# Performance work log

Measured on AMD Instinct MI355X. Metric: run time of the kernel, lower is better.

The kernel has to match this reference:

```python
import jax, jax.numpy as jnp
import numpy as np

D = 1024   # embedding_dim
H = 16     # head_num
DH = D // H
STD = 0.02


def setup_inputs() -> dict:
    key = jax.random.key(0)
    ks = jax.random.split(key, 8)
    B, S = 16, 2048
    inp = {
        "hidden_states": jax.random.normal(ks[0], (B, S, D), dtype=jnp.float32),
        "attention_mask": jnp.zeros((B, 1, S), dtype=jnp.float32),
        # nn.Linear params, stored as [in, out] for direct matmul
        "Wq": jax.random.normal(ks[1], (D, D), dtype=jnp.float32) * STD,
        "bq": jnp.zeros((D,), dtype=jnp.float32),
        "Wqa": jax.random.normal(ks[2], (D, H), dtype=jnp.float32) * STD,
        "bqa": jnp.zeros((H,), dtype=jnp.float32),
        "Wk": jax.random.normal(ks[3], (D, D), dtype=jnp.float32) * STD,
        "bk": jnp.zeros((D,), dtype=jnp.float32),
        "Wka": jax.random.normal(ks[4], (D, H), dtype=jnp.float32) * STD,
        "bka": jnp.zeros((H,), dtype=jnp.float32),
        "Wt": jax.random.normal(ks[5], (D, D), dtype=jnp.float32) * STD,
        "bt": jnp.zeros((D,), dtype=jnp.float32),
    }
    return inp


def reference(hidden_states, attention_mask, Wq, bq, Wqa, bqa, Wk, bk, Wka, bka, Wt, bt):
    B, S, _ = hidden_states.shape
    scale = 1.0 / np.sqrt(DH).astype(np.float32)

    mixed_q = hidden_states @ Wq + bq          # [B,S,D]
    mixed_k = hidden_states @ Wk + bk          # [B,S,D]

    # per-head query pooling scores: [B,S,H] -> [B,H,S]
    q_score = jnp.transpose(mixed_q @ Wqa + bqa, (0, 2, 1)) * scale + attention_mask
    q_weight = jax.nn.softmax(q_score, axis=-1)                 # [B,H,S]

    q_layer = mixed_q.reshape(B, S, H, DH).transpose(0, 2, 1, 3)  # [B,H,S,dh]
    pooled_q = jnp.einsum('bhs,bhsd->bhd', q_weight, q_layer)     # [B,H,dh]
    pooled_q_flat = pooled_q.reshape(B, 1, D)                     # [B,1,D] (head-major)

    # elementwise modulate keys with pooled query (broadcast, no repeat)
    mixed_qk = mixed_k * pooled_q_flat                            # [B,S,D]

    qk_score = jnp.transpose(mixed_qk @ Wka + bka, (0, 2, 1)) * scale + attention_mask
    qk_weight = jax.nn.softmax(qk_score, axis=-1)                 # [B,H,S]

    k_layer = mixed_qk.reshape(B, S, H, DH).transpose(0, 2, 1, 3)  # [B,H,S,dh]
    pooled_k = jnp.einsum('bhs,bhsd->bhd', qk_weight, k_layer)     # [B,H,dh]

    weighted = pooled_k[:, :, None, :] * q_layer                   # [B,H,S,dh]
    weighted = weighted.transpose(0, 2, 1, 3).reshape(B, S, D)     # [B,S,D]

    return weighted @ Wt + bt + mixed_q
```

## Files before the change

### kernel.cpp

```cpp
#include <hip/hip_runtime.h>
#include <hip/hip_bf16.h>
#include <stdint.h>

#define D_ 1024
#define H_ 16
#define DH_ 64
#define S_ 2048
#define B_ 16
static constexpr float SCALE = 0.125f;

typedef __bf16 bf16_t;
typedef __bf16 bf16x8 __attribute__((ext_vector_type(8)));
typedef __bf16 bf16x4 __attribute__((ext_vector_type(4)));
typedef float  f32x4  __attribute__((ext_vector_type(4)));

__device__ __forceinline__ void llds16(const void* g, void* l) {
  __builtin_amdgcn_global_load_lds(
      (const __attribute__((address_space(1))) void*)g,
      (__attribute__((address_space(3))) void*)l, 16, 0, 0);
}

__global__ __launch_bounds__(256)
void f32_to_bf16(const float* __restrict__ src, bf16_t* __restrict__ dst) {
  size_t base = ((size_t)blockIdx.x * 256 + threadIdx.x) * 8;
  f32x4 a = *(const f32x4*)&src[base];
  f32x4 b = *(const f32x4*)&src[base + 4];
  bf16x8 o;
#pragma unroll
  for (int i = 0; i < 4; ++i) { o[i] = (bf16_t)a[i]; o[4 + i] = (bf16_t)b[i]; }
  *(bf16x8*)&dst[base] = o;
}

__global__ __launch_bounds__(256)
void transpose1024_all(const float* __restrict__ s0, const float* __restrict__ s1,
                       const float* __restrict__ s2, bf16_t* __restrict__ d0,
                       bf16_t* __restrict__ d1, bf16_t* __restrict__ d2) {
  __shared__ bf16_t t[64][65];
  const float* src = (blockIdx.z == 0) ? s0 : (blockIdx.z == 1) ? s1 : s2;
  bf16_t* dst      = (blockIdx.z == 0) ? d0 : (blockIdx.z == 1) ? d1 : d2;
  const int n0 = blockIdx.x * 64, k0 = blockIdx.y * 64;
  const int r = threadIdx.x >> 4, c4 = (threadIdx.x & 15) * 4;
#pragma unroll
  for (int p = 0; p < 4; ++p) {
    int row = p * 16 + r;
    f32x4 f = *(const f32x4*)&src[(size_t)(k0 + row) * 1024 + n0 + c4];
#pragma unroll
    for (int i = 0; i < 4; ++i) t[row][c4 + i] = (bf16_t)f[i];
  }
  __syncthreads();
#pragma unroll
  for (int p = 0; p < 4; ++p) {
    int row = p * 16 + r;
    bf16x4 v;
#pragma unroll
    for (int i = 0; i < 4; ++i) v[i] = t[c4 + i][row];
    *(bf16x4*)&dst[(size_t)(n0 + row) * 1024 + k0 + c4] = v;
  }
}

__global__ __launch_bounds__(256)
void transpose_small_all(const float* __restrict__ sa, const float* __restrict__ sb,
                         bf16_t* __restrict__ da, bf16_t* __restrict__ db) {
  int g = blockIdx.x * 256 + threadIdx.x;
  const float* src = (g < 1024) ? sa : sb;
  bf16_t* dst      = (g < 1024) ? da : db;
  int k = g & 1023;
#pragma unroll
  for (int h = 0; h < H_; ++h) dst[h * 1024 + k] = (bf16_t)src[k * H_ + h];
}

__global__ __launch_bounds__(256, 2)
void gemm_qk(const bf16_t* __restrict__ A, const bf16_t* __restrict__ WqT,
             const bf16_t* __restrict__ WkT, const float* __restrict__ bq,
             const float* __restrict__ bk, bf16_t* __restrict__ mq,
             bf16_t* __restrict__ mk) {
  constexpr int K = 1024, N = 1024;
  __shared__ __align__(16) bf16_t lA[128 * 32];
  __shared__ __align__(16) bf16_t lB[128 * 32];
  __shared__ __align__(16) float est[4][16 * 68];
  const int tid = threadIdx.x;
  const int lane = tid & 63, wid = tid >> 6;
  const int wr = wid >> 1, wc = wid & 1;

  const int wgid = (blockIdx.x & 7) * 512 + (blockIdx.x >> 3);
  const int m0 = (wgid >> 4) * 128;
  const int nsel = wgid & 15;
  const int n0 = (nsel & 7) * 128;
  const bf16_t* BT = (nsel < 8) ? WqT : WkT;
  const float* bias = (nsel < 8) ? bq : bk;
  bf16_t* Cout = (nsel < 8) ? mq : mk;

  const int ar = lane & 15;
  const int kq = lane >> 4;

  int rowc[2], colc[2], dstoff[2];
#pragma unroll
  for (int j = 0; j < 2; ++j) {
    int c = j * 256 + tid;
    int row = c >> 2, s = c & 3;
    rowc[j] = row;
    colc[j] = (((s - (row >> 1)) & 3) << 3);
    dstoff[j] = c * 8;
  }

  f32x4 acc[4][4] = {};

  for (int k0 = 0; k0 < K; k0 += 32) {
#pragma unroll
    for (int j = 0; j < 2; ++j) {
      llds16(BT + (size_t)(n0 + rowc[j]) * K + k0 + colc[j], lB + dstoff[j]);
      llds16(A + (size_t)(m0 + rowc[j]) * K + k0 + colc[j], lA + dstoff[j]);
    }
    __syncthreads();
    bf16x8 af[4], bg[4];
#pragma unroll
    for (int m = 0; m < 4; ++m) {
      int r = wr * 64 + m * 16 + ar;
      af[m] = *(const bf16x8*)&lA[r * 32 + (((kq + (r >> 1)) & 3) << 3)];
    }
#pragma unroll
    for (int n = 0; n < 4; ++n) {
      int r = wc * 64 + n * 16 + ar;
      bg[n] = *(const bf16x8*)&lB[r * 32 + (((kq + (r >> 1)) & 3) << 3)];
    }
#pragma unroll
    for (int m = 0; m < 4; ++m)
#pragma unroll
      for (int n = 0; n < 4; ++n)
        acc[m][n] = __builtin_amdgcn_mfma_f32_16x16x32_bf16(af[m], bg[n], acc[m][n], 0, 0, 0);
    __syncthreads();
  }

  float* st = est[wid];
  const int erow = lane >> 2;
  const int ecol = (lane & 3) * 16;
  const int gcb = n0 + wc * 64;
  const int qrow = (lane >> 4) * 4;
  const int qcol = lane & 15;
  f32x4 bb[4];
#pragma unroll
  for (int q = 0; q < 4; ++q) bb[q] = *(const f32x4*)&bias[gcb + ecol + q * 4];
#pragma unroll
  for (int m = 0; m < 4; ++m) {
#pragma unroll
    for (int n = 0; n < 4; ++n)
#pragma unroll
      for (int j = 0; j < 4; ++j)
        st[(qrow + j) * 68 + n * 16 + qcol] = acc[m][n][j];
    asm volatile("s_waitcnt lgkmcnt(0)" ::: "memory");
    __builtin_amdgcn_sched_barrier(0);
    const int grow = m0 + wr * 64 + m * 16 + erow;
    f32x4 v[4];
#pragma unroll
    for (int q = 0; q < 4; ++q) v[q] = *(f32x4*)&st[erow * 68 + ecol + q * 4];
#pragma unroll
    for (int q = 0; q < 4; ++q)
#pragma unroll
      for (int i = 0; i < 4; ++i) v[q][i] += bb[q][i];
    bf16x8 o0, o1;
#pragma unroll
    for (int i = 0; i < 4; ++i) { o0[i] = (bf16_t)v[0][i]; o0[4 + i] = (bf16_t)v[1][i]; }
#pragma unroll
    for (int i = 0; i < 4; ++i) { o1[i] = (bf16_t)v[2][i]; o1[4 + i] = (bf16_t)v[3][i]; }
    bf16_t* op = Cout + (size_t)grow * N + gcb + ecol;
    *(bf16x8*)&op[0] = o0;
    *(bf16x8*)&op[8] = o1;
  }
}

__global__ __launch_bounds__(256, 2)
void gemm_out(const bf16_t* __restrict__ A, const bf16_t* __restrict__ BT,
              const float* __restrict__ bias, float* __restrict__ Cout,
              const bf16_t* __restrict__ resid, const float* __restrict__ pkA) {
  constexpr int K = 1024, N = 1024;
  __shared__ __align__(16) bf16_t lA[128 * 32];
  __shared__ __align__(16) bf16_t lB[128 * 32];
  __shared__ __align__(16) float est[4][16 * 68];
  const int tid = threadIdx.x;
  const int lane = tid & 63, wid = tid >> 6;
  const int wr = wid >> 1, wc = wid & 1;

  const int wgid = (blockIdx.x & 7) * 256 + (blockIdx.x >> 3);
  const int m0 = (wgid >> 3) * 128;
  const int n0 = (wgid & 7) * 128;
  const int b = m0 / S_;

  const int ar = lane & 15;
  const int kq = lane >> 4;

  int rowc[2], colc[2], dstoff[2];
#pragma unroll
  for (int j = 0; j < 2; ++j) {
    int c = j * 256 + tid;
    int row = c >> 2, s = c & 3;
    rowc[j] = row;
    colc[j] = (((s - (row >> 1)) & 3) << 3);
    dstoff[j] = c * 8;
  }

  f32x4 acc[4][4] = {};

  for (int k0 = 0; k0 < K; k0 += 32) {
#pragma unroll
    for (int j = 0; j < 2; ++j) {
      llds16(BT + (size_t)(n0 + rowc[j]) * K + k0 + colc[j], lB + dstoff[j]);
      bf16x8 v = *(const bf16x8*)(A + (size_t)(m0 + rowc[j]) * K + k0 + colc[j]);
      const float* pkp = pkA + b * D_ + k0 + colc[j];
      f32x4 p0 = *(const f32x4*)pkp;
      f32x4 p1 = *(const f32x4*)(pkp + 4);
      bf16x8 o;
#pragma unroll
      for (int i = 0; i < 4; ++i) {
        o[i]     = (bf16_t)((float)v[i] * p0[i]);
        o[4 + i] = (bf16_t)((float)v[4 + i] * p1[i]);
      }
      *(bf16x8*)&lA[dstoff[j]] = o;
    }
    __syncthreads();
    bf16x8 af[4], bg[4];
#pragma unroll
    for (int m = 0; m < 4; ++m) {
      int r = wr * 64 + m * 16 + ar;
      af[m] = *(const bf16x8*)&lA[r * 32 + (((kq + (r >> 1)) & 3) << 3)];
    }
#pragma unroll
    for (int n = 0; n < 4; ++n) {
      int r = wc * 64 + n * 16 + ar;
      bg[n] = *(const bf16x8*)&lB[r * 32 + (((kq + (r >> 1)) & 3) << 3)];
    }
#pragma unroll
    for (int m = 0; m < 4; ++m)
#pragma unroll
      for (int n = 0; n < 4; ++n)
        acc[m][n] = __builtin_amdgcn_mfma_f32_16x16x32_bf16(af[m], bg[n], acc[m][n], 0, 0, 0);
    __syncthreads();
  }

  float* st = est[wid];
  const int erow = lane >> 2;
  const int ecol = (lane & 3) * 16;
  const int gcb = n0 + wc * 64;
  const int qrow = (lane >> 4) * 4;
  const int qcol = lane & 15;
  f32x4 bb[4];
#pragma unroll
  for (int q = 0; q < 4; ++q) bb[q] = *(const f32x4*)&bias[gcb + ecol + q * 4];
#pragma unroll
  for (int m = 0; m < 4; ++m) {
#pragma unroll
    for (int n = 0; n < 4; ++n)
#pragma unroll
      for (int j = 0; j < 4; ++j)
        st[(qrow + j) * 68 + n * 16 + qcol] = acc[m][n][j];
    asm volatile("s_waitcnt lgkmcnt(0)" ::: "memory");
    __builtin_amdgcn_sched_barrier(0);
    const int grow = m0 + wr * 64 + m * 16 + erow;
    f32x4 v[4];
#pragma unroll
    for (int q = 0; q < 4; ++q) v[q] = *(f32x4*)&st[erow * 68 + ecol + q * 4];
#pragma unroll
    for (int q = 0; q < 4; ++q)
#pragma unroll
      for (int i = 0; i < 4; ++i) v[q][i] += bb[q][i];
    bf16x8 r0 = *(const bf16x8*)&resid[(size_t)grow * N + gcb + ecol];
    bf16x8 r1 = *(const bf16x8*)&resid[(size_t)grow * N + gcb + ecol + 8];
#pragma unroll
    for (int i = 0; i < 4; ++i) { v[0][i] += (float)r0[i]; v[1][i] += (float)r0[4 + i]; }
#pragma unroll
    for (int i = 0; i < 4; ++i) { v[2][i] += (float)r1[i]; v[3][i] += (float)r1[4 + i]; }
    float* op = Cout + (size_t)grow * N + gcb + ecol;
#pragma unroll
    for (int q = 0; q < 4; ++q) *(f32x4*)&op[q * 4] = v[q];
  }
}

template <int SCALED>
__global__ __launch_bounds__(256)
void score_kernel(const bf16_t* __restrict__ X, const bf16_t* __restrict__ WaT,
                  const float* __restrict__ ba, const float* __restrict__ mask,
                  const float* __restrict__ pq, float* __restrict__ scores) {
  const int lane = threadIdx.x & 63, wid = threadIdx.x >> 6;
  const int m0 = blockIdx.x * 64 + wid * 16;
  const int ar = lane & 15, ak = (lane >> 4) * 8;
  const int bb = m0 >> 11;
  f32x4 acc = {};
  for (int k0 = 0; k0 < D_; k0 += 32) {
    bf16x8 a = *(const bf16x8*)&X[(size_t)(m0 + ar) * D_ + k0 + ak];
    if (SCALED) {
      const float* pp = pq + bb * D_ + k0 + ak;
      f32x4 p0 = *(const f32x4*)pp;
      f32x4 p1 = *(const f32x4*)(pp + 4);
      bf16x8 a2;
#pragma unroll
      for (int i = 0; i < 4; ++i) {
        a2[i]     = (bf16_t)((float)a[i] * p0[i]);
        a2[4 + i] = (bf16_t)((float)a[4 + i] * p1[i]);
      }
      a = a2;
    }
    bf16x8 b = *(const bf16x8*)&WaT[(size_t)ar * D_ + k0 + ak];
    acc = __builtin_amdgcn_mfma_f32_16x16x32_bf16(a, b, acc, 0, 0, 0);
  }
  const int h = lane & 15;
  const int srow = m0 + (lane >> 4) * 4;
  const int s0 = srow - bb * S_;
  const float bah = ba[h];
  f32x4 mv = *(const f32x4*)&mask[(size_t)bb * S_ + s0];
  f32x4 outv;
#pragma unroll
  for (int j = 0; j < 4; ++j)
    outv[j] = (acc[j] + bah) * SCALE + mv[j];
  *(f32x4*)&scores[((size_t)(bb * H_ + h)) * S_ + s0] = outv;
}

__global__ __launch_bounds__(256)
void softmax_rows(const float* __restrict__ scores, float* __restrict__ wout) {
  __shared__ float rA[4], rB[4];
  const int tid = threadIdx.x, lane = tid & 63, wid = tid >> 6;
  const float* srow = scores + (size_t)blockIdx.x * S_;
  float* wrow = wout + (size_t)blockIdx.x * S_;
  f32x4 v0 = *(const f32x4*)&srow[tid * 4];
  f32x4 v1 = *(const f32x4*)&srow[1024 + tid * 4];
  float mx = fmaxf(fmaxf(fmaxf(v0[0], v0[1]), fmaxf(v0[2], v0[3])),
                   fmaxf(fmaxf(v1[0], v1[1]), fmaxf(v1[2], v1[3])));
#pragma unroll
  for (int o = 32; o; o >>= 1) mx = fmaxf(mx, __shfl_xor(mx, o));
  if (lane == 0) rA[wid] = mx;
  __syncthreads();
  mx = fmaxf(fmaxf(rA[0], rA[1]), fmaxf(rA[2], rA[3]));
  float sum = 0.f;
#pragma unroll
  for (int i = 0; i < 4; ++i) { v0[i] = __expf(v0[i] - mx); sum += v0[i]; }
#pragma unroll
  for (int i = 0; i < 4; ++i) { v1[i] = __expf(v1[i] - mx); sum += v1[i]; }
#pragma unroll
  for (int o = 32; o; o >>= 1) sum += __shfl_xor(sum, o);
  if (lane == 0) rB[wid] = sum;
  __syncthreads();
  sum = rB[0] + rB[1] + rB[2] + rB[3];
  const float inv = 1.0f / sum;
#pragma unroll
  for (int i = 0; i < 4; ++i) { v0[i] *= inv; v1[i] *= inv; }
  *(f32x4*)&wrow[tid * 4] = v0;
  *(f32x4*)&wrow[1024 + tid * 4] = v1;
}

__global__ __launch_bounds__(256)
void pool_partial(const bf16_t* __restrict__ X, const float* __restrict__ w,
                  float* __restrict__ partials) {
  __shared__ float sm[2][1024];
  const int tid = threadIdx.x;
  const int chunk = blockIdx.x, b = blockIdx.y;
  const int s0 = chunk * 32;
  const int dc = (tid & 127) * 8;
  const int sp = tid >> 7;
  const int h = dc >> 6;
  const float* wrow = w + ((size_t)b * H_ + h) * S_ + s0;
  const bf16_t* Xb = X + ((size_t)b * S_ + s0) * D_ + dc;
  float acc[8] = {};
  for (int s = sp; s < 32; s += 2) {
    bf16x8 xv = *(const bf16x8*)&Xb[(size_t)s * D_];
    float wt = wrow[s];
#pragma unroll
    for (int j = 0; j < 8; ++j) acc[j] += wt * (float)xv[j];
  }
#pragma unroll
  for (int j = 0; j < 8; ++j) sm[sp][dc + j] = acc[j];
  __syncthreads();
  const int d0 = tid * 4;
  f32x4 r;
#pragma unroll
  for (int j = 0; j < 4; ++j) r[j] = sm[0][d0 + j] + sm[1][d0 + j];
  *(f32x4*)&partials[((size_t)chunk * B_ + b) * D_ + d0] = r;
}

template <int SCALED>
__global__ __launch_bounds__(256)
void pool_reduce(const float* __restrict__ partials, const float* __restrict__ pq,
                 float* __restrict__ pooled) {
  const int idx = blockIdx.x * 256 + threadIdx.x;
  float s = 0.f;
#pragma unroll 8
  for (int c = 0; c < 64; ++c) s += partials[(size_t)c * (B_ * D_) + idx];
  if (SCALED) s *= pq[idx];
  pooled[idx] = s;
}

extern "C" void kernel_launch(void* const* d_in, const int* in_sizes, int n_in,
                              void* d_out, int out_size, void* d_ws, size_t ws_size,
                              hipStream_t stream) {
  const float* hs   = (const float*)d_in[0];
  const float* mask = (const float*)d_in[1];
  const float* Wq   = (const float*)d_in[2];
  const float* bq   = (const float*)d_in[3];
  const float* Wqa  = (const float*)d_in[4];
  const float* bqa  = (const float*)d_in[5];
  const float* Wk   = (const float*)d_in[6];
  const float* bk   = (const float*)d_in[7];
  const float* Wka  = (const float*)d_in[8];
  const float* bka  = (const float*)d_in[9];
  const float* Wt   = (const float*)d_in[10];
  const float* bt   = (const float*)d_in[11];

  char* ws = (char*)d_ws;
  float*  pq    = (float*)(ws + (64u << 10));
  float*  pk    = (float*)(ws + (128u << 10));
  bf16_t* WqaT  = (bf16_t*)(ws + (1u << 20));
  bf16_t* WkaT  = (bf16_t*)(ws + (1u << 20) + 32768);
  bf16_t* WqT   = (bf16_t*)(ws + (2u << 20));
  bf16_t* WkT   = (bf16_t*)(ws + (4u << 20));
  bf16_t* WtT   = (bf16_t*)(ws + (6u << 20));
  bf16_t* hsb   = (bf16_t*)(ws + (8u << 20));
  bf16_t* mq    = (bf16_t*)(ws + (8u << 20) + ((size_t)64 << 20));
  bf16_t* mk    = (bf16_t*)(ws + (8u << 20) + ((size_t)128 << 20));
  float* scores = (float*)(ws + (8u << 20) + ((size_t)192 << 20));
  float* wsm    = (float*)(ws + (8u << 20) + ((size_t)194 << 20));
  float* parts  = (float*)(ws + (8u << 20) + ((size_t)196 << 20));

  f32_to_bf16<<<16384, 256, 0, stream>>>(hs, hsb);
  transpose1024_all<<<dim3(16, 16, 3), 256, 0, stream>>>(Wq, Wk, Wt, WqT, WkT, WtT);
  transpose_small_all<<<8, 256, 0, stream>>>(Wqa, Wka, WqaT, WkaT);

  gemm_qk<<<4096, 256, 0, stream>>>(hsb, WqT, WkT, bq, bk, mq, mk);

  score_kernel<0><<<512, 256, 0, stream>>>(mq, WqaT, bqa, mask, nullptr, scores);
  softmax_rows<<<256, 256, 0, stream>>>(scores, wsm);
  pool_partial<<<dim3(64, 16), 256, 0, stream>>>(mq, wsm, parts);
  pool_reduce<0><<<64, 256, 0, stream>>>(parts, nullptr, pq);

  score_kernel<1><<<512, 256, 0, stream>>>(mk, WkaT, bka, mask, pq, scores);
  softmax_rows<<<256, 256, 0, stream>>>(scores, wsm);
  pool_partial<<<dim3(64, 16), 256, 0, stream>>>(mk, wsm, parts);
  pool_reduce<1><<<64, 256, 0, stream>>>(parts, pq, pk);

  gemm_out<<<2048, 256, 0, stream>>>(mq, WtT, bt, (float*)d_out, mq, pk);
}
```

Measured before the change: 400.2 us.

## Fold pooled query into per-batch key-score weights and merge prep kernels

Uses (k*pq)·Wka = k·(pq∘Wka) to build a per-batch scaled Wka in pool_reduce, so the second score kernel no longer multiplies every key element by the pooled query inside its K loop. It also merges the hidden-state conversion and the three weight-transpose kernels into one prep_all launch, cutting launch count. The rounding point moves (the product is rounded into bf16 weights instead of into the activations), which slightly changes numerics.

```diff
diff --git a/kernel.cpp b/kernel.cpp
--- a/kernel.cpp
+++ b/kernel.cpp
@@ -21,52 +21,60 @@
 }
 
 __global__ __launch_bounds__(256)
-void f32_to_bf16(const float* __restrict__ src, bf16_t* __restrict__ dst) {
-  size_t base = ((size_t)blockIdx.x * 256 + threadIdx.x) * 8;
-  f32x4 a = *(const f32x4*)&src[base];
-  f32x4 b = *(const f32x4*)&src[base + 4];
-  bf16x8 o;
-#pragma unroll
-  for (int i = 0; i < 4; ++i) { o[i] = (bf16_t)a[i]; o[4 + i] = (bf16_t)b[i]; }
-  *(bf16x8*)&dst[base] = o;
-}
-
-__global__ __launch_bounds__(256)
-void transpose1024_all(const float* __restrict__ s0, const float* __restrict__ s1,
-                       const float* __restrict__ s2, bf16_t* __restrict__ d0,
-                       bf16_t* __restrict__ d1, bf16_t* __restrict__ d2) {
+void prep_all(const float* __restrict__ Wq, const float* __restrict__ Wk,
+              const float* __restrict__ Wt, const float* __restrict__ Wqa,
+              const float* __restrict__ Wka, const float* __restrict__ hs,
+              bf16_t* __restrict__ WqT, bf16_t* __restrict__ WkT,
+              bf16_t* __restrict__ WtT, bf16_t* __restrict__ WqaT,
+              bf16_t* __restrict__ WkaT, bf16_t* __restrict__ hsb) {
   __shared__ bf16_t t[64][65];
-  const float* src = (blockIdx.z == 0) ? s0 : (blockIdx.z == 1) ? s1 : s2;
-  bf16_t* dst      = (blockIdx.z == 0) ? d0 : (blockIdx.z == 1) ? d1 : d2;
-  const int n0 = blockIdx.x * 64, k0 = blockIdx.y * 64;
-  const int r = threadIdx.x >> 4, c4 = (threadIdx.x & 15) * 4;
-#pragma unroll
-  for (int p = 0; p < 4; ++p) {
-    int row = p * 16 + r;
-    f32x4 f = *(const f32x4*)&src[(size_t)(k0 + row) * 1024 + n0 + c4];
-#pragma unroll
-    for (int i = 0; i < 4; ++i) t[row][c4 + i] = (bf16_t)f[i];
-  }
-  __syncthreads();
-#pragma unroll
-  for (int p = 0; p < 4; ++p) {
-    int row = p * 16 + r;
-    bf16x4 v;
-#pragma unroll
-    for (int i = 0; i < 4; ++i) v[i] = t[c4 + i][row];
-    *(bf16x4*)&dst[(size_t)(n0 + row) * 1024 + k0 + c4] = v;
-  }
-}
-
-__global__ __launch_bounds__(256)
-void transpose_small_all(const float* __restrict__ sa, const float* __restrict__ sb,
-                         bf16_t* __restrict__ da, bf16_t* __restrict__ db) {
-  int g = blockIdx.x * 256 + threadIdx.x;
-  const float* src = (g < 1024) ? sa : sb;
-  bf16_t* dst      = (g < 1024) ? da : db;
-  int k = g & 1023;
-#pragma unroll
-  for (int h = 0; h < H_; ++h) dst[h * 1024 + k] = (bf16_t)src[k * H_ + h];
+  const int z = blockIdx.z;
+  const int tid = threadIdx.x;
+  if (z < 3) {
+    const float* src = (z == 0) ? Wq : (z == 1) ? Wk : Wt;
+    bf16_t* dst      = (z == 0) ? WqT : (z == 1) ? WkT : WtT;
+    const int n0 = blockIdx.x * 64, k0 = blockIdx.y * 64;
+    const int r = tid >> 4, c4 = (tid & 15) * 4;
+#pragma unroll
+    for (int p = 0; p < 4; ++p) {
+      int row = p * 16 + r;
+      f32x4 f = *(const f32x4*)&src[(size_t)(k0 + row) * 1024 + n0 + c4];
+#pragma unroll
+      for (int i = 0; i < 4; ++i) t[row][c4 + i] = (bf16_t)f[i];
+    }
+    __syncthreads();
+#pragma unroll
+    for (int p = 0; p < 4; ++p) {
+      int row = p * 16 + r;
+      bf16x4 v;
+#pragma unroll
+      for (int i = 0; i < 4; ++i) v[i] = t[c4 + i][row];
+      *(bf16x4*)&dst[(size_t)(n0 + row) * 1024 + k0 + c4] = v;
+    }
+  } else if (z == 3) {
+    int g = (blockIdx.y * 16 + blockIdx.x) * 256 + tid;
+    if (g < 2048) {
+      const float* src = (g < 1024) ? Wqa : Wka;
+      bf16_t* dst      = (g < 1024) ? WqaT : WkaT;
+      int k = g & 1023;
+#pragma unroll
+      for (int h = 0; h < H_; ++h) dst[h * 1024 + k] = (bf16_t)src[k * H_ + h];
+    }
+  } else {
+    const int slice = z - 4;
+    const int fb = blockIdx.y * 16 + blockIdx.x;
+    const size_t tbase = ((size_t)slice * 256 + fb) * 256 + tid;
+#pragma unroll
+    for (int i = 0; i < 4; ++i) {
+      size_t e = (tbase + (size_t)i * 1048576) * 8;
+      f32x4 a = *(const f32x4*)&hs[e];
+      f32x4 b = *(const f32x4*)&hs[e + 4];
+      bf16x8 o;
+#pragma unroll
+      for (int j = 0; j < 4; ++j) { o[j] = (bf16_t)a[j]; o[4 + j] = (bf16_t)b[j]; }
+      *(bf16x8*)&hsb[e] = o;
+    }
+  }
 }
 
 __global__ __launch_bounds__(256, 2)
@@ -274,31 +282,20 @@
   }
 }
 
-template <int SCALED>
+template <int PER_B>
 __global__ __launch_bounds__(256)
 void score_kernel(const bf16_t* __restrict__ X, const bf16_t* __restrict__ WaT,
                   const float* __restrict__ ba, const float* __restrict__ mask,
-                  const float* __restrict__ pq, float* __restrict__ scores) {
+                  float* __restrict__ scores) {
   const int lane = threadIdx.x & 63, wid = threadIdx.x >> 6;
   const int m0 = blockIdx.x * 64 + wid * 16;
   const int ar = lane & 15, ak = (lane >> 4) * 8;
   const int bb = m0 >> 11;
+  const bf16_t* Wb = WaT + (PER_B ? (size_t)bb * H_ * D_ : 0);
   f32x4 acc = {};
   for (int k0 = 0; k0 < D_; k0 += 32) {
     bf16x8 a = *(const bf16x8*)&X[(size_t)(m0 + ar) * D_ + k0 + ak];
-    if (SCALED) {
-      const float* pp = pq + bb * D_ + k0 + ak;
-      f32x4 p0 = *(const f32x4*)pp;
-      f32x4 p1 = *(const f32x4*)(pp + 4);
-      bf16x8 a2;
-#pragma unroll
-      for (int i = 0; i < 4; ++i) {
-        a2[i]     = (bf16_t)((float)a[i] * p0[i]);
-        a2[4 + i] = (bf16_t)((float)a[4 + i] * p1[i]);
-      }
-      a = a2;
-    }
-    bf16x8 b = *(const bf16x8*)&WaT[(size_t)ar * D_ + k0 + ak];
+    bf16x8 b = *(const bf16x8*)&Wb[(size_t)ar * D_ + k0 + ak];
     acc = __builtin_amdgcn_mfma_f32_16x16x32_bf16(a, b, acc, 0, 0, 0);
   }
   const int h = lane & 15;
@@ -374,16 +371,23 @@
   *(f32x4*)&partials[((size_t)chunk * B_ + b) * D_ + d0] = r;
 }
 
-template <int SCALED>
+template <int MODE>
 __global__ __launch_bounds__(256)
 void pool_reduce(const float* __restrict__ partials, const float* __restrict__ pq,
-                 float* __restrict__ pooled) {
+                 const bf16_t* __restrict__ WkaT, float* __restrict__ pooled,
+                 bf16_t* __restrict__ wka_s) {
   const int idx = blockIdx.x * 256 + threadIdx.x;
   float s = 0.f;
 #pragma unroll 8
   for (int c = 0; c < 64; ++c) s += partials[(size_t)c * (B_ * D_) + idx];
-  if (SCALED) s *= pq[idx];
+  if (MODE == 1) s *= pq[idx];
   pooled[idx] = s;
+  if (MODE == 0) {
+    const int b = idx >> 10, d = idx & 1023;
+#pragma unroll
+    for (int h = 0; h < H_; ++h)
+      wka_s[((size_t)b * H_ + h) * D_ + d] = (bf16_t)(s * (float)WkaT[h * D_ + d]);
+  }
 }
 
 extern "C" void kernel_launch(void* const* d_in, const int* in_sizes, int n_in,
@@ -405,6 +409,7 @@
   char* ws = (char*)d_ws;
   float*  pq    = (float*)(ws + (64u << 10));
   float*  pk    = (float*)(ws + (128u << 10));
+  bf16_t* wka_s = (bf16_t*)(ws + (256u << 10));
   bf16_t* WqaT  = (bf16_t*)(ws + (1u << 20));
   bf16_t* WkaT  = (bf16_t*)(ws + (1u << 20) + 32768);
   bf16_t* WqT   = (bf16_t*)(ws + (2u << 20));
@@ -417,21 +422,20 @@
   float* wsm    = (float*)(ws + (8u << 20) + ((size_t)194 << 20));
   float* parts  = (float*)(ws + (8u << 20) + ((size_t)196 << 20));
 
-  f32_to_bf16<<<16384, 256, 0, stream>>>(hs, hsb);
-  transpose1024_all<<<dim3(16, 16, 3), 256, 0, stream>>>(Wq, Wk, Wt, WqT, WkT, WtT);
-  transpose_small_all<<<8, 256, 0, stream>>>(Wqa, Wka, WqaT, WkaT);
+  prep_all<<<dim3(16, 16, 20), 256, 0, stream>>>(Wq, Wk, Wt, Wqa, Wka, hs,
+                                                 WqT, WkT, WtT, WqaT, WkaT, hsb);
 
   gemm_qk<<<4096, 256, 0, stream>>>(hsb, WqT, WkT, bq, bk, mq, mk);
 
-  score_kernel<0><<<512, 256, 0, stream>>>(mq, WqaT, bqa, mask, nullptr, scores);
+  score_kernel<0><<<512, 256, 0, stream>>>(mq, WqaT, bqa, mask, scores);
   softmax_rows<<<256, 256, 0, stream>>>(scores, wsm);
   pool_partial<<<dim3(64, 16), 256, 0, stream>>>(mq, wsm, parts);
-  pool_reduce<0><<<64, 256, 0, stream>>>(parts, nullptr, pq);
-
-  score_kernel<1><<<512, 256, 0, stream>>>(mk, WkaT, bka, mask, pq, scores);
+  pool_reduce<0><<<64, 256, 0, stream>>>(parts, nullptr, WkaT, pq, wka_s);
+
+  score_kernel<1><<<512, 256, 0, stream>>>(mk, wka_s, bka, mask, scores);
   softmax_rows<<<256, 256, 0, stream>>>(scores, wsm);
   pool_partial<<<dim3(64, 16), 256, 0, stream>>>(mk, wsm, parts);
-  pool_reduce<1><<<64, 256, 0, stream>>>(parts, pq, pk);
+  pool_reduce<1><<<64, 256, 0, stream>>>(parts, pq, nullptr, pk, nullptr);
 
   gemm_out<<<2048, 256, 0, stream>>>(mq, WtT, bt, (float*)d_out, mq, pk);
 }
```

Result: no change. 395.9 us (-1.1%).
